# Optimization experiments

Hardware: AMD Instinct MI355X
Metric: run time of the kernel (lower is better)

## Reference

```python
import jax, jax.numpy as jnp
import numpy as np

B, T, D, E, I = 8, 8192, 128, 8, 16
EPS = 1e-5


def setup_inputs() -> dict:
    key = jax.random.key(0)
    ks = jax.random.split(key, 6)
    return {
        "x": jax.random.normal(ks[0], (B, T, D), dtype=jnp.float32),
        "ln_g": jnp.ones((D,), dtype=jnp.float32),
        "ln_b": jnp.zeros((D,), dtype=jnp.float32),
        "gate_w": jax.random.normal(ks[1], (D, E), dtype=jnp.float32) * (1.0 / np.sqrt(D)),
        "gate_b": jnp.zeros((E,), dtype=jnp.float32),
        "w1": jax.random.normal(ks[2], (E, D, I), dtype=jnp.float32),
        "w2": jax.random.normal(ks[3], (E, I, D), dtype=jnp.float32),
    }


def reference(x, ln_g, ln_b, gate_w, gate_b, w1, w2):
    # LayerNorm (torch default eps=1e-5)
    mu = jnp.mean(x, axis=-1, keepdims=True)
    var = jnp.mean(jnp.square(x - mu), axis=-1, keepdims=True)
    x_norm = (x - mu) * jax.lax.rsqrt(var + EPS) * ln_g + ln_b

    # Dense gating + softmax routing
    gating_logits = x_norm @ gate_w + gate_b          # [B,T,E]
    routing_weights = jax.nn.softmax(gating_logits, axis=-1)

    # All-expert FFN: small batched GEMMs (torch F.gelu default = exact erf)
    y = jax.nn.gelu(jnp.einsum('btc,eci->btei', x_norm, w1), approximate=False)
    moe_experts_out = jnp.einsum('btei,eic->btec', y, w2)  # [B,T,E,D]
    moe_agg = jnp.einsum('btec,bte->btc', moe_experts_out, routing_weights)

    return (x + moe_agg, gating_logits, moe_experts_out)
```

## Files before the change

### kernel.cpp

```cpp
#include <hip/hip_runtime.h>
#include <math.h>

#define O1_OFF 8388608
#define O2_OFF 8912896

#define WS_W2T 32768
#define WS_GFR 65536

typedef __attribute__((ext_vector_type(8))) short short8;
typedef __attribute__((ext_vector_type(4))) float f32x4;

static __device__ __forceinline__ unsigned short f2bf(float f) {
    unsigned u = __builtin_bit_cast(unsigned, f);
    u = (u + 0x7fffu + ((u >> 16) & 1u)) >> 16;
    return (unsigned short)u;
}

static __device__ __forceinline__ int swz(int row, int chunk) {
    return row * 256 + ((chunk ^ (row & 7)) << 4);
}

static __device__ __forceinline__ int tswz(int row, int col) {
    int chunk = (col >> 3) ^ ((row >> 1) & 6);
    return row * 256 + (chunk << 4) + ((col & 7) << 1);
}

static __device__ __forceinline__ void bar_lds() {
    asm volatile("s_waitcnt lgkmcnt(0)" ::: "memory");
    __builtin_amdgcn_s_barrier();
    asm volatile("" ::: "memory");
}

static __device__ __forceinline__ void fence_lds() {
    asm volatile("s_waitcnt lgkmcnt(0)" ::: "memory");
}

__global__ __launch_bounds__(256) void moe_prep(
    const float* __restrict__ gate_w, const float* __restrict__ w1,
    const float* __restrict__ w2, char* __restrict__ ws)
{
    const int t = threadIdx.x;
    const int b = blockIdx.x;
    if (b < 4) {
        const int p = t & 127, ch = t >> 7;
        const float* w1b = w1 + (p >> 4) * 2048 + (p & 15);
        #pragma unroll
        for (int q = 0; q < 2; ++q) {
            int cc = 2 * b + q;
            short8 v;
            #pragma unroll
            for (int j = 0; j < 8; ++j)
                v[j] = (short)f2bf(w1b[(ch * 64 + cc * 8 + j) * 16]);
            *(short8*)(ws + swz(p, ch * 8 + cc)) = v;
        }
        if (b == 0 && t < 64) {
            const int col = t & 15, ak = t >> 4;
            #pragma unroll
            for (int ks = 0; ks < 4; ++ks) {
                short8 v;
                #pragma unroll
                for (int j = 0; j < 8; ++j) {
                    float f = (col < 8) ? gate_w[(32 * ks + 8 * ak + j) * 8 + col] : 0.0f;
                    v[j] = (short)f2bf(f);
                }
                *(short8*)(ws + WS_GFR + t * 64 + ks * 16) = v;
            }
        }
    } else {
        const int e2 = t >> 5, colq = (t & 31) * 4;
        const int cc = b - 4;
        const int c = colq + cc;
        const float* w2b = w2 + e2 * 2048 + c;
        unsigned pkc[8];
        #pragma unroll
        for (int q = 0; q < 8; ++q) pkc[q] = 0u;
        #pragma unroll
        for (int i = 0; i < 16; ++i)
            pkc[i >> 1] |= (unsigned)f2bf(w2b[i * 128]) << ((i & 1) * 16);
        const int rc = e2 * 128 + c;
        const int a = (c >> 2) & 3;
        *(uint4*)(ws + WS_W2T + (((rc * 2 + 0) ^ a) << 4)) =
            make_uint4(pkc[0], pkc[1], pkc[2], pkc[3]);
        *(uint4*)(ws + WS_W2T + (((rc * 2 + 1) ^ a) << 4)) =
            make_uint4(pkc[4], pkc[5], pkc[6], pkc[7]);
    }
}

__global__ __launch_bounds__(256, 2) void moe_fused(
    const float* __restrict__ x, const float* __restrict__ ln_g,
    const float* __restrict__ ln_b, const float* __restrict__ gate_b,
    const char* __restrict__ wsw, float* __restrict__ out)
{
    __shared__ __align__(16) char smem[67584];
    char* pXY = smem;
    char* pW  = smem + 16384;
    char* pTR = smem + 49152;
    float* pRW = (float*)(smem + 65536);

    const int t = threadIdx.x;
    const int l = t & 63;
    const int w = t >> 6;
    const int tok0 = blockIdx.x * 64;

    const int colq = (t & 31) * 4;
    const int rsub = t >> 5;

    const int rb = w * 16;
    const int col = l & 15;
    const int ak = l >> 4;
    const int arow = rb + col;

    float4 xv[8];
    {
        const float* xb = x + (size_t)tok0 * 128;
        #pragma unroll
        for (int s = 0; s < 8; ++s)
            xv[s] = *(const float4*)(xb + s * 1024 + t * 4);
    }
    float4 g4 = *(const float4*)(ln_g + colq);
    float4 b4 = *(const float4*)(ln_b + colq);

    #pragma unroll
    for (int k = 0; k < 8; ++k)
        *(uint4*)(pW + t * 16 + k * 4096) = *(const uint4*)(wsw + t * 16 + k * 4096);

    short8 gfr[4];
    #pragma unroll
    for (int ks = 0; ks < 4; ++ks)
        gfr[ks] = *(const short8*)(wsw + WS_GFR + l * 64 + ks * 16);
    float4 gb4 = *(const float4*)(gate_b + (ak & 1) * 4);

    #pragma unroll
    for (int s = 0; s < 8; ++s) {
        float4 v = xv[s];
        float sm = v.x + v.y + v.z + v.w;
        float sq = v.x*v.x + v.y*v.y + v.z*v.z + v.w*v.w;
        #pragma unroll
        for (int m = 1; m < 32; m <<= 1) {
            sm += __shfl_xor(sm, m, 64);
            sq += __shfl_xor(sq, m, 64);
        }
        float mu = sm * (1.0f / 128.0f);
        float var = sq * (1.0f / 128.0f) - mu * mu;
        float rs = rsqrtf(var + 1e-5f);
        float n0 = (v.x - mu) * rs * g4.x + b4.x;
        float n1 = (v.y - mu) * rs * g4.y + b4.y;
        float n2 = (v.z - mu) * rs * g4.z + b4.z;
        float n3 = (v.w - mu) * rs * g4.w + b4.w;
        unsigned lo = (unsigned)f2bf(n0) | ((unsigned)f2bf(n1) << 16);
        unsigned hi = (unsigned)f2bf(n2) | ((unsigned)f2bf(n3) << 16);
        unsigned long long dvv = (unsigned long long)lo | ((unsigned long long)hi << 32);
        int row = s * 8 + rsub;
        *(unsigned long long*)(pXY + swz(row, colq >> 3) + (colq & 7) * 2) = dvv;
    }

    bar_lds();

    const f32x4 zero4 = {0.f, 0.f, 0.f, 0.f};
    const short8 zfrag = {0, 0, 0, 0, 0, 0, 0, 0};

    short8 afr[4];
    #pragma unroll
    for (int ks = 0; ks < 4; ++ks)
        afr[ks] = *(const short8*)(pXY + swz(arow, ks * 4 + ak));

    f32x4 accg = zero4;
    #pragma unroll
    for (int ks = 0; ks < 4; ++ks)
        accg = __builtin_amdgcn_mfma_f32_16x16x32_bf16(gfr[ks], afr[ks], accg, 0, 0, 0);

    const size_t trow = (size_t)(tok0 + arow);
    {
        float lg0 = accg[0] + gb4.x;
        float lg1 = accg[1] + gb4.y;
        float lg2 = accg[2] + gb4.z;
        float lg3 = accg[3] + gb4.w;
        if (ak < 2) {
            f32x4 lgv = {lg0, lg1, lg2, lg3};
            *(f32x4*)(out + O1_OFF + trow * 8 + ak * 4) = lgv;
        }
        float mx = fmaxf(fmaxf(lg0, lg1), fmaxf(lg2, lg3));
        mx = fmaxf(mx, __shfl_xor(mx, 16, 64));
        float ex0 = __expf(lg0 - mx), ex1 = __expf(lg1 - mx);
        float ex2 = __expf(lg2 - mx), ex3 = __expf(lg3 - mx);
        float sm = ex0 + ex1 + ex2 + ex3;
        sm += __shfl_xor(sm, 16, 64);
        float inv = 1.0f / sm;
        if (ak < 2) {
            f32x4 pv = {ex0 * inv, ex1 * inv, ex2 * inv, ex3 * inv};
            *(f32x4*)(pRW + arow * 8 + ak * 4) = pv;
        }
    }

    f32x4 accb[8];
    #pragma unroll
    for (int nt = 0; nt < 8; ++nt) accb[nt] = zero4;
    #pragma unroll
    for (int ks = 0; ks < 4; ++ks)
        #pragma unroll
        for (int nt = 0; nt < 8; ++nt) {
            short8 wfr = *(const short8*)(pW + swz(nt * 16 + col, ks * 4 + ak));
            accb[nt] = __builtin_amdgcn_mfma_f32_16x16x32_bf16(wfr, afr[ks], accb[nt], 0, 0, 0);
        }

    #pragma unroll
    for (int nt = 0; nt < 8; ++nt) {
        float y0 = accb[nt][0], y1 = accb[nt][1], y2 = accb[nt][2], y3 = accb[nt][3];
        y0 = 0.5f * y0 * (1.0f + erff(y0 * 0.70710678118654752f));
        y1 = 0.5f * y1 * (1.0f + erff(y1 * 0.70710678118654752f));
        y2 = 0.5f * y2 * (1.0f + erff(y2 * 0.70710678118654752f));
        y3 = 0.5f * y3 * (1.0f + erff(y3 * 0.70710678118654752f));
        unsigned lo = (unsigned)f2bf(y0) | ((unsigned)f2bf(y1) << 16);
        unsigned hi = (unsigned)f2bf(y2) | ((unsigned)f2bf(y3) << 16);
        unsigned long long dv = (unsigned long long)lo | ((unsigned long long)hi << 32);
        *(unsigned long long*)(pXY + swz(arow, nt * 2 + (ak >> 1)) + (ak & 1) * 8) = dv;
    }

    bar_lds();

    #pragma unroll
    for (int k = 0; k < 8; ++k)
        *(uint4*)(pW + t * 16 + k * 4096) = *(const uint4*)(wsw + WS_W2T + t * 16 + k * 4096);

    bar_lds();

    f32x4 agg[8];
    #pragma unroll
    for (int nt = 0; nt < 8; ++nt) agg[nt] = zero4;

    #pragma unroll
    for (int e = 0; e < 8; ++e) {
        float rwe[4];
        #pragma unroll
        for (int r = 0; r < 4; ++r)
            rwe[r] = pRW[(rb + ak * 4 + r) * 8 + e];
        short8 alo = *(const short8*)(pXY + swz(arow, 2 * e + (ak & 1)));
        short8 af = (ak < 2) ? alo : zfrag;
        f32x4 ot[8];
        #pragma unroll
        for (int nt = 0; nt < 8; ++nt) {
            int c = nt * 16 + col;
            int rc = e * 128 + c;
            int a = (c >> 2) & 3;
            short8 blo = *(const short8*)(pW + (((rc * 2 + (ak & 1)) ^ a) << 4));
            short8 bf = (ak < 2) ? blo : zfrag;
            ot[nt] = __builtin_amdgcn_mfma_f32_16x16x32_bf16(af, bf, zero4, 0, 0, 0);
            #pragma unroll
            for (int r = 0; r < 4; ++r)
                agg[nt][r] += rwe[r] * ot[nt][r];
        }
        #pragma unroll
        for (int nt = 0; nt < 8; ++nt)
            #pragma unroll
            for (int r = 0; r < 4; ++r)
                *(unsigned short*)(pTR + tswz(rb + ak * 4 + r, nt * 16 + col)) = f2bf(ot[nt][r]);
        fence_lds();
        #pragma unroll
        for (int i2 = 0; i2 < 8; ++i2) {
            int row = rb + i2 * 2 + (l >> 5);
            int c0 = (l & 31) * 4;
            unsigned long long raw = *(const unsigned long long*)(pTR + tswz(row, c0));
            unsigned lo = (unsigned)raw, hi = (unsigned)(raw >> 32);
            f32x4 v;
            v[0] = __builtin_bit_cast(float, lo << 16);
            v[1] = __builtin_bit_cast(float, lo & 0xffff0000u);
            v[2] = __builtin_bit_cast(float, hi << 16);
            v[3] = __builtin_bit_cast(float, hi & 0xffff0000u);
            __builtin_nontemporal_store(v,
                (f32x4*)(out + O2_OFF + (size_t)(tok0 + row) * 1024 + e * 128 + c0));
        }
        asm volatile("" ::: "memory");
    }

    bar_lds();

    #pragma unroll
    for (int nt = 0; nt < 8; ++nt) {
        int c = nt * 16 + col;
        #pragma unroll
        for (int r = 0; r < 4; ++r) {
            int row = rb + ak * 4 + r;
            *(float*)(pW + row * 512 + ((c << 2) ^ ((row & 4) << 2))) = agg[nt][r];
        }
    }

    bar_lds();

    #pragma unroll
    for (int s = 0; s < 8; ++s) {
        int row = s * 8 + rsub;
        f32x4 a4 = *(const f32x4*)(pW + row * 512 + ((colq << 2) ^ ((row & 4) << 2)));
        f32x4 o;
        o[0] = xv[s].x + a4[0];
        o[1] = xv[s].y + a4[1];
        o[2] = xv[s].z + a4[2];
        o[3] = xv[s].w + a4[3];
        __builtin_nontemporal_store(o,
            (f32x4*)(out + (size_t)(tok0 + row) * 128 + colq));
    }
}

extern "C" void kernel_launch(void* const* d_in, const int* in_sizes, int n_in,
                              void* d_out, int out_size, void* d_ws, size_t ws_size,
                              hipStream_t stream) {
    const float* x      = (const float*)d_in[0];
    const float* ln_g   = (const float*)d_in[1];
    const float* ln_b   = (const float*)d_in[2];
    const float* gate_w = (const float*)d_in[3];
    const float* gate_b = (const float*)d_in[4];
    const float* w1     = (const float*)d_in[5];
    const float* w2     = (const float*)d_in[6];
    float* out = (float*)d_out;
    char* ws = (char*)d_ws;
    (void)in_sizes; (void)n_in; (void)out_size; (void)ws_size;
    moe_prep<<<dim3(8), dim3(256), 0, stream>>>(gate_w, w1, w2, ws);
    moe_fused<<<dim3(1024), dim3(256), 0, stream>>>(x, ln_g, ln_b, gate_b, ws, out);
}
```

Baseline: 80.33 us.

## Shrink LDS footprint to fit three blocks per CU by splitting W2 staging

Cuts the static shared-memory buffer from about 66KB to 50KB and raises launch bounds to 3 blocks per CU. To fit, the transposed W2 weights are staged in two halves of four experts each, with an extra barrier and reload between them. The first-stage W1 tile and the final aggregation buffer now spill over into the scratch transpose region. Higher occupancy should hide more of the store-bound expert-output writes, at the cost of a tighter register budget (possible spills), extra barriers, and a partial tail wave over 1024 blocks.

```diff
diff --git a/kernel.cpp b/kernel.cpp
--- a/kernel.cpp
+++ b/kernel.cpp
@@ -86,16 +86,16 @@
     }
 }
 
-__global__ __launch_bounds__(256, 2) void moe_fused(
+__global__ __launch_bounds__(256, 3) void moe_fused(
     const float* __restrict__ x, const float* __restrict__ ln_g,
     const float* __restrict__ ln_b, const float* __restrict__ gate_b,
     const char* __restrict__ wsw, float* __restrict__ out)
 {
-    __shared__ __align__(16) char smem[67584];
+    __shared__ __align__(16) char smem[51200];
     char* pXY = smem;
-    char* pW  = smem + 16384;
-    char* pTR = smem + 49152;
-    float* pRW = (float*)(smem + 65536);
+    char* pWT = smem + 16384;
+    char* pTR = smem + 32768;
+    float* pRW = (float*)(smem + 49152);
 
     const int t = threadIdx.x;
     const int l = t & 63;
@@ -122,7 +122,7 @@
 
     #pragma unroll
     for (int k = 0; k < 8; ++k)
-        *(uint4*)(pW + t * 16 + k * 4096) = *(const uint4*)(wsw + t * 16 + k * 4096);
+        *(uint4*)(pWT + t * 16 + k * 4096) = *(const uint4*)(wsw + t * 16 + k * 4096);
 
     short8 gfr[4];
     #pragma unroll
@@ -199,7 +199,7 @@
     for (int ks = 0; ks < 4; ++ks)
         #pragma unroll
         for (int nt = 0; nt < 8; ++nt) {
-            short8 wfr = *(const short8*)(pW + swz(nt * 16 + col, ks * 4 + ak));
+            short8 wfr = *(const short8*)(pWT + swz(nt * 16 + col, ks * 4 + ak));
             accb[nt] = __builtin_amdgcn_mfma_f32_16x16x32_bf16(wfr, afr[ks], accb[nt], 0, 0, 0);
         }
 
@@ -219,8 +219,8 @@
     bar_lds();
 
     #pragma unroll
-    for (int k = 0; k < 8; ++k)
-        *(uint4*)(pW + t * 16 + k * 4096) = *(const uint4*)(wsw + WS_W2T + t * 16 + k * 4096);
+    for (int k = 0; k < 4; ++k)
+        *(uint4*)(pWT + t * 16 + k * 4096) = *(const uint4*)(wsw + WS_W2T + t * 16 + k * 4096);
 
     bar_lds();
 
@@ -229,47 +229,59 @@
     for (int nt = 0; nt < 8; ++nt) agg[nt] = zero4;
 
     #pragma unroll
-    for (int e = 0; e < 8; ++e) {
-        float rwe[4];
-        #pragma unroll
-        for (int r = 0; r < 4; ++r)
-            rwe[r] = pRW[(rb + ak * 4 + r) * 8 + e];
-        short8 alo = *(const short8*)(pXY + swz(arow, 2 * e + (ak & 1)));
-        short8 af = (ak < 2) ? alo : zfrag;
-        f32x4 ot[8];
-        #pragma unroll
-        for (int nt = 0; nt < 8; ++nt) {
-            int c = nt * 16 + col;
-            int rc = e * 128 + c;
-            int a = (c >> 2) & 3;
-            short8 blo = *(const short8*)(pW + (((rc * 2 + (ak & 1)) ^ a) << 4));
-            short8 bf = (ak < 2) ? blo : zfrag;
-            ot[nt] = __builtin_amdgcn_mfma_f32_16x16x32_bf16(af, bf, zero4, 0, 0, 0);
+    for (int pass = 0; pass < 2; ++pass) {
+        if (pass == 1) {
+            bar_lds();
+            #pragma unroll
+            for (int k = 0; k < 4; ++k)
+                *(uint4*)(pWT + t * 16 + k * 4096) =
+                    *(const uint4*)(wsw + WS_W2T + 16384 + t * 16 + k * 4096);
+            bar_lds();
+        }
+        #pragma unroll
+        for (int el = 0; el < 4; ++el) {
+            int e = pass * 4 + el;
+            float rwe[4];
             #pragma unroll
             for (int r = 0; r < 4; ++r)
-                agg[nt][r] += rwe[r] * ot[nt][r];
-        }
-        #pragma unroll
-        for (int nt = 0; nt < 8; ++nt)
-            #pragma unroll
-            for (int r = 0; r < 4; ++r)
-                *(unsigned short*)(pTR + tswz(rb + ak * 4 + r, nt * 16 + col)) = f2bf(ot[nt][r]);
-        fence_lds();
-        #pragma unroll
-        for (int i2 = 0; i2 < 8; ++i2) {
-            int row = rb + i2 * 2 + (l >> 5);
-            int c0 = (l & 31) * 4;
-            unsigned long long raw = *(const unsigned long long*)(pTR + tswz(row, c0));
-            unsigned lo = (unsigned)raw, hi = (unsigned)(raw >> 32);
-            f32x4 v;
-            v[0] = __builtin_bit_cast(float, lo << 16);
-            v[1] = __builtin_bit_cast(float, lo & 0xffff0000u);
-            v[2] = __builtin_bit_cast(float, hi << 16);
-            v[3] = __builtin_bit_cast(float, hi & 0xffff0000u);
-            __builtin_nontemporal_store(v,
-                (f32x4*)(out + O2_OFF + (size_t)(tok0 + row) * 1024 + e * 128 + c0));
-        }
-        asm volatile("" ::: "memory");
+                rwe[r] = pRW[(rb + ak * 4 + r) * 8 + e];
+            short8 alo = *(const short8*)(pXY + swz(arow, 2 * e + (ak & 1)));
+            short8 af = (ak < 2) ? alo : zfrag;
+            f32x4 ot[8];
+            #pragma unroll
+            for (int nt = 0; nt < 8; ++nt) {
+                int c = nt * 16 + col;
+                int rc = el * 128 + c;
+                int a = (c >> 2) & 3;
+                short8 blo = *(const short8*)(pWT + (((rc * 2 + (ak & 1)) ^ a) << 4));
+                short8 bf = (ak < 2) ? blo : zfrag;
+                ot[nt] = __builtin_amdgcn_mfma_f32_16x16x32_bf16(af, bf, zero4, 0, 0, 0);
+                #pragma unroll
+                for (int r = 0; r < 4; ++r)
+                    agg[nt][r] += rwe[r] * ot[nt][r];
+            }
+            #pragma unroll
+            for (int nt = 0; nt < 8; ++nt)
+                #pragma unroll
+                for (int r = 0; r < 4; ++r)
+                    *(unsigned short*)(pTR + tswz(rb + ak * 4 + r, nt * 16 + col)) = f2bf(ot[nt][r]);
+            fence_lds();
+            #pragma unroll
+            for (int i2 = 0; i2 < 8; ++i2) {
+                int row = rb + i2 * 2 + (l >> 5);
+                int c0 = (l & 31) * 4;
+                unsigned long long raw = *(const unsigned long long*)(pTR + tswz(row, c0));
+                unsigned lo = (unsigned)raw, hi = (unsigned)(raw >> 32);
+                f32x4 v;
+                v[0] = __builtin_bit_cast(float, lo << 16);
+                v[1] = __builtin_bit_cast(float, lo & 0xffff0000u);
+                v[2] = __builtin_bit_cast(float, hi << 16);
+                v[3] = __builtin_bit_cast(float, hi & 0xffff0000u);
+                __builtin_nontemporal_store(v,
+                    (f32x4*)(out + O2_OFF + (size_t)(tok0 + row) * 1024 + e * 128 + c0));
+            }
+            asm volatile("" ::: "memory");
+        }
     }
 
     bar_lds();
@@ -280,7 +292,7 @@
         #pragma unroll
         for (int r = 0; r < 4; ++r) {
             int row = rb + ak * 4 + r;
-            *(float*)(pW + row * 512 + ((c << 2) ^ ((row & 4) << 2))) = agg[nt][r];
+            *(float*)(pWT + row * 512 + ((c << 2) ^ ((row & 4) << 2))) = agg[nt][r];
         }
     }
 
@@ -289,7 +301,7 @@
     #pragma unroll
     for (int s = 0; s < 8; ++s) {
         int row = s * 8 + rsub;
-        f32x4 a4 = *(const f32x4*)(pW + row * 512 + ((colq << 2) ^ ((row & 4) << 2)));
+        f32x4 a4 = *(const f32x4*)(pWT + row * 512 + ((colq << 2) ^ ((row & 4) << 2)));
         f32x4 o;
         o[0] = xv[s].x + a4[0];
         o[1] = xv[s].y + a4[1];
```

Result: slower. 122.1 us (+52.0%).
